# Optimization experiments

Hardware: AMD Instinct MI355X
Metric: run time of the kernel (lower is better)

The kernel has to match this reference:

```python
import jax, jax.numpy as jnp
import numpy as np

# Production-scale dims (GraspNet-style CloudCrop)
B, N, C, NS = 8, 1024, 256, 32          # batch, seed points (= npoint), feat dim, nsample
RADIUS, HMIN, HMAX = 0.05, -0.02, 0.04
EPS = 1e-5


def setup_inputs() -> dict:
    key = jax.random.key(0)
    ks = jax.random.split(key, 8)
    # seed points in a 0.2m cube -> cylinder of r=0.05, h=0.06 holds ~60 pts on avg
    seed_xyz_graspable = jax.random.uniform(ks[0], (B, N, 3), dtype=jnp.float32) * 0.2
    seed_features_graspable = jax.random.normal(ks[1], (B, C, N), dtype=jnp.float32)
    # random proper-ish rotation matrices via batched QR (orthonormal columns)
    q, _ = jnp.linalg.qr(jax.random.normal(ks[2], (B, N, 3, 3), dtype=jnp.float32))
    vp_rot = q
    cin = 3 + C
    # kaiming_normal for 1x1 convs (fan_in = cin), BN -> no conv bias
    W1 = jax.random.normal(ks[3], (256, cin), dtype=jnp.float32) * np.sqrt(2.0 / cin)
    W2 = jax.random.normal(ks[4], (256, 256), dtype=jnp.float32) * np.sqrt(2.0 / 256)
    g1 = jnp.ones((256,), jnp.float32); b1 = jnp.zeros((256,), jnp.float32)
    g2 = jnp.ones((256,), jnp.float32); b2 = jnp.zeros((256,), jnp.float32)
    return dict(seed_xyz_graspable=seed_xyz_graspable,
                seed_features_graspable=seed_features_graspable,
                vp_rot=vp_rot, W1=W1, g1=g1, b1=b1, W2=W2, g2=g2, b2=b2)


def _cylinder_query_idx(xyz, new_xyz, rot):
    # local coords: x_rot = R^T (p - c); rot flattened row-major in the original,
    # so local_k = sum_m rot[m, k] * diff_m  ==  einsum(diff, rot)
    diff = xyz[:, None, :, :] - new_xyz[:, :, None, :]          # (B, P, N, 3)
    local = jnp.einsum('bpnm,bpmk->bpnk', diff, rot)            # (B, P, N, 3)
    d2 = local[..., 1] ** 2 + local[..., 2] ** 2
    mask = (d2 < RADIUS ** 2) & (local[..., 0] > HMIN) & (local[..., 0] < HMAX)
    # first NS in-cylinder indices in original point order; empty slots -> index 0
    order = jnp.argsort(~mask, axis=-1)[..., :NS]               # stable sort
    valid = jnp.take_along_axis(mask, order, axis=-1)
    return jnp.where(valid, order, 0)                           # (B, P, NS) int32


def _conv_bn_relu(x, W, g, b):
    # 1x1 conv as channel GEMM, BatchNorm2d (training stats), ReLU
    y = jnp.einsum('bcps,oc->bops', x, W)                       # (B, O, P, S)
    mu = y.mean(axis=(0, 2, 3), keepdims=True)
    var = y.var(axis=(0, 2, 3), keepdims=True)
    y = (y - mu) * jax.lax.rsqrt(var + EPS)
    y = y * g[None, :, None, None] + b[None, :, None, None]
    return jax.nn.relu(y)


def reference(seed_xyz_graspable, seed_features_graspable, vp_rot,
              W1, g1, b1, W2, g2, b2):
    xyz, feats, rot = seed_xyz_graspable, seed_features_graspable, vp_rot
    idx = _cylinder_query_idx(xyz, xyz, rot)                    # centers == seeds
    # group xyz: gather, recenter, normalize by radius, rotate into cylinder frame
    gx = jax.vmap(lambda p, i: p[i])(xyz, idx)                  # (B, P, NS, 3)
    gx = (gx - xyz[:, :, None, :]) / RADIUS
    gx = jnp.einsum('bpsm,bpmk->bpsk', gx, rot)                 # rotate_xyz
    gf = jax.vmap(lambda f, i: f[:, i])(feats, idx)             # (B, C, P, NS)
    x = jnp.concatenate([gx.transpose(0, 3, 1, 2), gf], axis=1)  # (B, 3+C, P, NS)
    x = _conv_bn_relu(x, W1, g1, b1)
    x = _conv_bn_relu(x, W2, g2, b2)
    return x.max(axis=-1)                                        # (B, 256, P)
```

## Files before the change

kernel.cpp:

```cpp
#include <hip/hip_runtime.h>
#include <hip/hip_bf16.h>

#define DB 8
#define DN 1024
#define DP 1024
#define DC 256
#define DNS 32
#define DBP (DB * DP)
#define K1 288
#define K2 256
#define XS 296
#define YS 258
#define ROWS 128
#define NG (DBP / 4)
#define NK1 (K1 / 32)
#define NK2 (K2 / 32)

constexpr float kRadius = 0.05f;
constexpr float kR2 = kRadius * kRadius;
constexpr float kHmin = -0.02f;
constexpr float kHmax = 0.04f;
constexpr float kEps = 1e-5f;
constexpr float kInvCnt = 1.0f / (float)(DB * DP * DNS);

typedef __bf16 bf16x8 __attribute__((ext_vector_type(8)));
typedef float f32x4 __attribute__((ext_vector_type(4)));
static_assert(sizeof(bf16x8) == 16, "bf16x8 must be 16B");

constexpr size_t OF_FEATST = 0;
constexpr size_t OF_W1B  = OF_FEATST + (size_t)DB * DN * DC / 2;
constexpr size_t OF_W2B  = OF_W1B + (size_t)DC * K1 / 2;
constexpr size_t OF_IDX  = OF_W2B + (size_t)DC * K2 / 2;
constexpr size_t OF_GX   = OF_IDX + (size_t)DBP * DNS;
constexpr size_t OF_PART = OF_GX + (size_t)DBP * DNS * 3;
constexpr size_t OF_YMAX = OF_PART + (size_t)DBP * DC * 2;
constexpr size_t OF_YMIN = OF_YMAX + (size_t)DBP * DC;
constexpr size_t OF_BN1  = OF_YMIN + (size_t)DBP * DC;
constexpr size_t OF_BN2  = OF_BN1 + 512;
constexpr size_t OF_CNTZ = OF_BN2 + 512;
constexpr size_t OF_GWZ  = OF_CNTZ + (size_t)64 * DN;
constexpr size_t OF_GG64 = OF_GWZ + (size_t)64 * 3 * DN;
constexpr size_t OF_YPRT = OF_GG64 + 1024;

__device__ inline ushort f2b(float x) {
  union { __hip_bfloat16 h; ushort u; } c;
  c.h = __float2bfloat16(x);
  return c.u;
}
__device__ inline float b2f(ushort u) {
  union { uint u; float f; } c;
  c.u = (uint)u << 16;
  return c.f;
}

__global__ __launch_bounds__(256)
void k_prep(const float* __restrict__ f, uint* __restrict__ ftb,
            const float* __restrict__ W1, ushort* __restrict__ W1b,
            const float* __restrict__ W2, ushort* __restrict__ W2b) {
  __shared__ float t[32][33];
  int blk = blockIdx.x;
  int tid = threadIdx.x;
  if (blk < 2048) {
    int ct = blk & 7, nt = (blk >> 3) & 31, b = blk >> 8;
    int tx = tid & 31, ty = tid >> 5;
#pragma unroll
    for (int k = 0; k < 4; ++k) {
      int c = ct * 32 + ty + k * 8;
      t[ty + k * 8][tx] = f[((size_t)b * DC + c) * DN + nt * 32 + tx];
    }
    __syncthreads();
    uint* dst = ftb + (size_t)b * DN * (DC / 2);
#pragma unroll
    for (int it = 0; it < 2; ++it) {
      int idx = it * 256 + tid;
      int nl = idx >> 4, cp = idx & 15;
      uint v = (uint)f2b(t[2 * cp][nl]) | ((uint)f2b(t[2 * cp + 1][nl]) << 16);
      dst[(size_t)(nt * 32 + nl) * (DC / 2) + ct * 16 + cp] = v;
    }
  } else if (blk < 2336) {
    int gid = (blk - 2048) * 256 + tid;
    if (gid < DC * K1) {
      int o = gid / K1, kp = gid - o * K1;
      float v = 0.f;
      if (kp < 256) v = W1[o * 259 + 3 + kp];
      else if (kp < 259) v = W1[o * 259 + (kp - 256)];
      W1b[gid] = f2b(v);
    }
  } else {
    int gid = (blk - 2336) * 256 + tid;
    if (gid < DC * K2) W2b[gid] = f2b(W2[gid]);
  }
}

__global__ void k_query(const float* __restrict__ xyz, const float* __restrict__ rot,
                        int* __restrict__ idxp, float* __restrict__ gxp) {
  int bp = blockIdx.x;
  int b = bp >> 10;
  int lane = threadIdx.x;
  __shared__ int sidx[DNS];
  __shared__ float srot[9], sc[3];
  if (lane < DNS) sidx[lane] = 0;
  if (lane < 9) srot[lane] = rot[(size_t)bp * 9 + lane];
  if (lane < 3) sc[lane] = xyz[(size_t)bp * 3 + lane];
  __syncthreads();
  float r00 = srot[0], r01 = srot[1], r02 = srot[2];
  float r10 = srot[3], r11 = srot[4], r12 = srot[5];
  float r20 = srot[6], r21 = srot[7], r22 = srot[8];
  float cx = sc[0], cy = sc[1], cz = sc[2];
  const float* xb = xyz + (size_t)b * DN * 3;
  int cnt = 0;
  for (int ch = 0; ch < DN / 64 && cnt < DNS; ++ch) {
    int n = ch * 64 + lane;
    float dx = xb[n * 3 + 0] - cx, dy = xb[n * 3 + 1] - cy, dz = xb[n * 3 + 2] - cz;
    float lx = dx * r00 + dy * r10 + dz * r20;
    float ly = dx * r01 + dy * r11 + dz * r21;
    float lz = dx * r02 + dy * r12 + dz * r22;
    bool m = (ly * ly + lz * lz < kR2) && (lx > kHmin) && (lx < kHmax);
    unsigned long long bal = __ballot(m);
    int rank = cnt + __popcll(bal & ((1ull << lane) - 1ull));
    if (m && rank < DNS) sidx[rank] = n;
    cnt += __popcll(bal);
  }
  __syncthreads();
  if (lane < DNS) {
    int j = sidx[lane];
    idxp[(size_t)bp * DNS + lane] = j;
    float gx = (xb[j * 3 + 0] - cx) / kRadius;
    float gy = (xb[j * 3 + 1] - cy) / kRadius;
    float gz = (xb[j * 3 + 2] - cz) / kRadius;
    float* gp = gxp + ((size_t)bp * DNS + lane) * 3;
    gp[0] = gx * r00 + gy * r10 + gz * r20;
    gp[1] = gx * r01 + gy * r11 + gz * r21;
    gp[2] = gx * r02 + gy * r12 + gz * r22;
  }
}

__global__ __launch_bounds__(256)
void k_count(const int* __restrict__ idxp, const float* __restrict__ gxp,
             float* __restrict__ cntz, float* __restrict__ gwz,
             float* __restrict__ gg64) {
  __shared__ float h0[DN], h1[DN], h2[DN], h3[DN];
  int t = threadIdx.x;
  int blk = blockIdx.x;
  int b = blk >> 3, s = blk & 7;
  for (int i = t; i < DN; i += 256) {
    h0[i] = 0.f; h1[i] = 0.f; h2[i] = 0.f; h3[i] = 0.f;
  }
  __syncthreads();
  float p[9] = {0.f, 0.f, 0.f, 0.f, 0.f, 0.f, 0.f, 0.f, 0.f};
#pragma unroll
  for (int r = 0; r < 16; ++r) {
    int sid = blk * 4096 + r * 256 + t;
    int j = idxp[sid];
    const float* g = gxp + (size_t)sid * 3;
    float g0 = g[0], g1 = g[1], g2 = g[2];
    atomicAdd(&h0[j], 1.f);
    atomicAdd(&h1[j], g0);
    atomicAdd(&h2[j], g1);
    atomicAdd(&h3[j], g2);
    p[0] += g0 * g0; p[1] += g0 * g1; p[2] += g0 * g2;
    p[3] += g1 * g1; p[4] += g1 * g2; p[5] += g2 * g2;
    p[6] += g0; p[7] += g1; p[8] += g2;
  }
  __syncthreads();
  for (int i = t; i < DN; i += 256) {
    cntz[((size_t)b * 8 + s) * DN + i] = h0[i];
    gwz[(((size_t)b * 8 + s) * 3 + 0) * DN + i] = h1[i];
    gwz[(((size_t)b * 8 + s) * 3 + 1) * DN + i] = h2[i];
    gwz[(((size_t)b * 8 + s) * 3 + 2) * DN + i] = h3[i];
  }
  __shared__ float sgg[4][9];
#pragma unroll
  for (int v = 0; v < 9; ++v) {
    float sv = p[v];
#pragma unroll
    for (int m = 1; m < 64; m <<= 1) sv += __shfl_xor(sv, m, 64);
    if ((t & 63) == 0) sgg[t >> 6][v] = sv;
  }
  __syncthreads();
  if (t < 9) gg64[blk * 16 + t] = sgg[0][t] + sgg[1][t] + sgg[2][t] + sgg[3][t];
}

__global__ __launch_bounds__(256)
void k_ygemm(const uint4* __restrict__ ftb, const ushort* __restrict__ W1b,
             const float* __restrict__ W1, const float* __restrict__ cntz,
             const float* __restrict__ gwz, float2* __restrict__ ypart) {
  __shared__ ushort x_lds[ROWS * XS];
  __shared__ float c_lds[ROWS];
  __shared__ float g_lds[3][ROWS];
  __shared__ float wg_lds[DC][3];

  const int nb = blockIdx.x;
  const int b = nb >> 3;
  const int n0 = (nb & 7) * ROWS;
  const int tid = threadIdx.x;
  const int lane = tid & 63;
  const int wv = tid >> 6;
  const int l15 = lane & 15;
  const int l4 = lane >> 4;

  {
    const uint4* src = ftb + ((size_t)b * DN + n0) * (DC / 8);
    for (int idx = tid; idx < ROWS * 32; idx += 256) {
      int rrow = idx >> 5, col = idx & 31;
      ((uint4*)(x_lds + (size_t)rrow * XS))[col] = src[rrow * 32 + col];
    }
  }
  if (tid < ROWS) {
    float c = 0.f, g0 = 0.f, g1 = 0.f, g2 = 0.f;
#pragma unroll
    for (int s = 0; s < 8; ++s) {
      c += cntz[((size_t)b * 8 + s) * DN + n0 + tid];
      g0 += gwz[(((size_t)b * 8 + s) * 3 + 0) * DN + n0 + tid];
      g1 += gwz[(((size_t)b * 8 + s) * 3 + 1) * DN + n0 + tid];
      g2 += gwz[(((size_t)b * 8 + s) * 3 + 2) * DN + n0 + tid];
    }
    c_lds[tid] = c; g_lds[0][tid] = g0; g_lds[1][tid] = g1; g_lds[2][tid] = g2;
  }
  {
    wg_lds[tid][0] = W1[tid * 259 + 0];
    wg_lds[tid][1] = W1[tid * 259 + 1];
    wg_lds[tid][2] = W1[tid * 259 + 2];
  }
  __syncthreads();

  f32x4 acc[4][8];
#pragma unroll
  for (int t = 0; t < 4; ++t)
#pragma unroll
    for (int st = 0; st < 8; ++st)
#pragma unroll
      for (int r = 0; r < 4; ++r) acc[t][st][r] = 0.f;

  const int o0 = wv * 64;
  const ushort* xbase = x_lds + (size_t)l15 * XS + l4 * 8;
  {
    const ushort* wrow[4];
#pragma unroll
    for (int t = 0; t < 4; ++t)
      wrow[t] = W1b + (size_t)(o0 + t * 16 + l15) * K1 + l4 * 8;
#pragma unroll
    for (int ks = 0; ks < 8; ++ks) {
      bf16x8 bx[8], aw[4];
#pragma unroll
      for (int st = 0; st < 8; ++st)
        bx[st] = *(const bf16x8*)(xbase + (size_t)st * 16 * XS + ks * 32);
#pragma unroll
      for (int t = 0; t < 4; ++t) aw[t] = *(const bf16x8*)(wrow[t] + ks * 32);
#pragma unroll
      for (int st = 0; st < 8; ++st)
#pragma unroll
        for (int t = 0; t < 4; ++t)
          acc[t][st] = __builtin_amdgcn_mfma_f32_16x16x32_bf16(aw[t], bx[st],
                                                               acc[t][st], 0, 0, 0);
    }
  }

  float cn[8], h0[8], h1[8], h2[8];
#pragma unroll
  for (int st = 0; st < 8; ++st) {
    int n = st * 16 + l15;
    cn[st] = c_lds[n]; h0[st] = g_lds[0][n]; h1[st] = g_lds[1][n]; h2[st] = g_lds[2][n];
  }
#pragma unroll
  for (int t = 0; t < 4; ++t) {
#pragma unroll
    for (int r = 0; r < 4; ++r) {
      int o = o0 + t * 16 + l4 * 4 + r;
      float wg0 = wg_lds[o][0], wg1 = wg_lds[o][1], wg2 = wg_lds[o][2];
      float s = 0.f, q = 0.f;
#pragma unroll
      for (int st = 0; st < 8; ++st) {
        float Y = acc[t][st][r];
        float h = wg0 * h0[st] + wg1 * h1[st] + wg2 * h2[st];
        s = fmaf(cn[st], Y, s);
        q += cn[st] * Y * Y + 2.f * Y * h;
      }
#pragma unroll
      for (int m = 1; m < 16; m <<= 1) {
        s += __shfl_xor(s, m, 64);
        q += __shfl_xor(q, m, 64);
      }
      if (l15 == 0) ypart[(size_t)nb * DC + o] = make_float2(s, q);
    }
  }
}

__global__ __launch_bounds__(256)
void k_bn1f(const float2* __restrict__ ypart, const float* __restrict__ gg64,
            const float* __restrict__ W1, const float* __restrict__ gam,
            const float* __restrict__ bet, float* __restrict__ bn) {
  __shared__ float ggs[9];
  int t = threadIdx.x;
  if (t < 9) {
    float s = 0.f;
    for (int blk = 0; blk < 64; ++blk) s += gg64[blk * 16 + t];
    ggs[t] = s;
  }
  __syncthreads();
  float s = 0.f, q = 0.f;
  for (int nb = 0; nb < 64; ++nb) {
    float2 v = ypart[(size_t)nb * DC + t];
    s += v.x; q += v.y;
  }
  float wg0 = W1[t * 259 + 0], wg1 = W1[t * 259 + 1], wg2 = W1[t * 259 + 2];
  s += wg0 * ggs[6] + wg1 * ggs[7] + wg2 * ggs[8];
  q += wg0 * wg0 * ggs[0] + 2.f * wg0 * wg1 * ggs[1] + 2.f * wg0 * wg2 * ggs[2] +
       wg1 * wg1 * ggs[3] + 2.f * wg1 * wg2 * ggs[4] + wg2 * wg2 * ggs[5];
  float mu = s * kInvCnt;
  float var = q * kInvCnt - mu * mu;
  var = var < 0.f ? 0.f : var;
  float sc = gam[t] * rsqrtf(var + kEps);
  bn[t] = sc;
  bn[DC + t] = bet[t] - mu * sc;
}

__global__ __launch_bounds__(256, 2)
void k_gemm_full(const uint4* __restrict__ ftb, const ushort* __restrict__ W1b,
                 const ushort* __restrict__ W2b, const int* __restrict__ idxp,
                 const float* __restrict__ gxp, const float* __restrict__ bn1,
                 float2* __restrict__ part, float* __restrict__ ymax,
                 float* __restrict__ ymin) {
  __shared__ ushort x_lds[ROWS * XS];
  __shared__ float bn_lds[2 * DC];

  const int grp = blockIdx.x;
  const int bp0 = grp * 4;
  const int b = bp0 >> 10;
  const int tid = threadIdx.x;
  const int lane = tid & 63;
  const int wv = tid >> 6;
  const int l15 = lane & 15;
  const int l4 = lane >> 4;

  for (int i = tid; i < 2 * DC; i += 256) bn_lds[i] = bn1[i];

  {
    int q = tid & 7;
#pragma unroll
    for (int rep = 0; rep < 4; ++rep) {
      int s = (tid >> 3) + rep * 32;
      int j = idxp[(size_t)bp0 * DNS + s];
      const uint4* src = ftb + (size_t)(b * DN + j) * (DC / 8);
      uint4* dst = (uint4*)(x_lds + (size_t)s * XS);
#pragma unroll
      for (int k = 0; k < 4; ++k) dst[q + 8 * k] = src[q + 8 * k];
    }
  }
  if (tid < ROWS) {
    const float* g = gxp + ((size_t)bp0 * DNS + tid) * 3;
    uint a0 = (uint)f2b(g[0]) | ((uint)f2b(g[1]) << 16);
    uint a1 = (uint)f2b(g[2]);
    uint4* drow = (uint4*)(x_lds + (size_t)tid * XS + 256);
    drow[0] = make_uint4(a0, a1, 0u, 0u);
    drow[1] = make_uint4(0u, 0u, 0u, 0u);
    drow[2] = make_uint4(0u, 0u, 0u, 0u);
    drow[3] = make_uint4(0u, 0u, 0u, 0u);
  }
  __syncthreads();

  f32x4 acc[4][8];
#pragma unroll
  for (int t = 0; t < 4; ++t)
#pragma unroll
    for (int st = 0; st < 8; ++st)
#pragma unroll
      for (int r = 0; r < 4; ++r) acc[t][st][r] = 0.f;

  const int o0 = wv * 64;
  const ushort* xbase = x_lds + (size_t)l15 * XS + l4 * 8;

  {
    const ushort* wrow[4];
#pragma unroll
    for (int t = 0; t < 4; ++t)
      wrow[t] = W1b + (size_t)(o0 + t * 16 + l15) * K1 + l4 * 8;
    bf16x8 aw[4];
#pragma unroll
    for (int t = 0; t < 4; ++t) aw[t] = *(const bf16x8*)(wrow[t]);
#pragma unroll
    for (int ks = 0; ks < NK1; ++ks) {
      bf16x8 bx[8];
#pragma unroll
      for (int st = 0; st < 8; ++st)
        bx[st] = *(const bf16x8*)(xbase + (size_t)st * 16 * XS + ks * 32);
      bf16x8 an[4];
      if (ks + 1 < NK1) {
#pragma unroll
        for (int t = 0; t < 4; ++t)
          an[t] = *(const bf16x8*)(wrow[t] + (ks + 1) * 32);
      }
      __builtin_amdgcn_s_setprio(1);
#pragma unroll
      for (int st = 0; st < 8; ++st)
#pragma unroll
        for (int t = 0; t < 4; ++t)
          acc[t][st] = __builtin_amdgcn_mfma_f32_16x16x32_bf16(aw[t], bx[st],
                                                               acc[t][st], 0, 0, 0);
      __builtin_amdgcn_s_setprio(0);
      if (ks + 1 < NK1) {
#pragma unroll
        for (int t = 0; t < 4; ++t) aw[t] = an[t];
      }
    }
  }

  __syncthreads();
#pragma unroll
  for (int t = 0; t < 4; ++t) {
    int ob = o0 + t * 16 + l4 * 4;
    float sc0 = bn_lds[ob + 0], sh0 = bn_lds[DC + ob + 0];
    float sc1 = bn_lds[ob + 1], sh1 = bn_lds[DC + ob + 1];
    float sc2 = bn_lds[ob + 2], sh2 = bn_lds[DC + ob + 2];
    float sc3 = bn_lds[ob + 3], sh3 = bn_lds[DC + ob + 3];
#pragma unroll
    for (int st = 0; st < 8; ++st) {
      float v0 = fmaxf(fmaf(acc[t][st][0], sc0, sh0), 0.f);
      float v1 = fmaxf(fmaf(acc[t][st][1], sc1, sh1), 0.f);
      float v2 = fmaxf(fmaf(acc[t][st][2], sc2, sh2), 0.f);
      float v3 = fmaxf(fmaf(acc[t][st][3], sc3, sh3), 0.f);
      uint2 pk = make_uint2((uint)f2b(v0) | ((uint)f2b(v1) << 16),
                            (uint)f2b(v2) | ((uint)f2b(v3) << 16));
      int s = st * 16 + l15;
      *(uint2*)(x_lds + (size_t)s * XS + ob) = pk;
      acc[t][st][0] = 0.f; acc[t][st][1] = 0.f;
      acc[t][st][2] = 0.f; acc[t][st][3] = 0.f;
    }
  }
  __syncthreads();

  {
    const ushort* wrow[4];
#pragma unroll
    for (int t = 0; t < 4; ++t)
      wrow[t] = W2b + (size_t)(o0 + t * 16 + l15) * K2 + l4 * 8;
    bf16x8 aw[4];
#pragma unroll
    for (int t = 0; t < 4; ++t) aw[t] = *(const bf16x8*)(wrow[t]);
#pragma unroll
    for (int ks = 0; ks < NK2; ++ks) {
      bf16x8 bx[8];
#pragma unroll
      for (int st = 0; st < 8; ++st)
        bx[st] = *(const bf16x8*)(xbase + (size_t)st * 16 * XS + ks * 32);
      bf16x8 an[4];
      if (ks + 1 < NK2) {
#pragma unroll
        for (int t = 0; t < 4; ++t)
          an[t] = *(const bf16x8*)(wrow[t] + (ks + 1) * 32);
      }
      __builtin_amdgcn_s_setprio(1);
#pragma unroll
      for (int st = 0; st < 8; ++st)
#pragma unroll
        for (int t = 0; t < 4; ++t)
          acc[t][st] = __builtin_amdgcn_mfma_f32_16x16x32_bf16(aw[t], bx[st],
                                                               acc[t][st], 0, 0, 0);
      __builtin_amdgcn_s_setprio(0);
      if (ks + 1 < NK2) {
#pragma unroll
        for (int t = 0; t < 4; ++t) aw[t] = an[t];
      }
    }
  }

  __syncthreads();
#pragma unroll
  for (int t = 0; t < 4; ++t) {
    int ob = o0 + t * 16 + l4 * 4;
#pragma unroll
    for (int st = 0; st < 8; ++st) {
      uint2 pk = make_uint2(
          (uint)f2b(acc[t][st][0]) | ((uint)f2b(acc[t][st][1]) << 16),
          (uint)f2b(acc[t][st][2]) | ((uint)f2b(acc[t][st][3]) << 16));
      int s = st * 16 + l15;
      *(uint2*)(x_lds + (size_t)s * YS + ob) = pk;
    }
  }
  __syncthreads();
  {
    const ushort* col = x_lds + tid;
    float s = 0.f, q = 0.f;
#pragma unroll
    for (int p = 0; p < 4; ++p) {
      float mx = -3.4e38f, mn = 3.4e38f;
#pragma unroll 8
      for (int i = 0; i < DNS; ++i) {
        float v = b2f(col[(size_t)(p * DNS + i) * YS]);
        s += v; q += v * v;
        mx = fmaxf(mx, v); mn = fminf(mn, v);
      }
      ymax[(size_t)(bp0 + p) * DC + tid] = mx;
      ymin[(size_t)(bp0 + p) * DC + tid] = mn;
    }
    part[(size_t)grp * DC + tid] = make_float2(s, q);
  }
}

__global__ void k_reduce_bn(const float* __restrict__ part, const float* __restrict__ gam,
                            const float* __restrict__ bet, float* __restrict__ bn) {
  int o = blockIdx.x, tid = threadIdx.x;
  __shared__ float ss[256], sq[256];
  float s = 0.f, q = 0.f;
  const float2* pp = (const float2*)part;
  for (int g = tid; g < NG; g += 256) {
    float2 v = pp[(size_t)g * DC + o];
    s += v.x; q += v.y;
  }
  ss[tid] = s; sq[tid] = q;
  __syncthreads();
  for (int w = 128; w > 0; w >>= 1) {
    if (tid < w) { ss[tid] += ss[tid + w]; sq[tid] += sq[tid + w]; }
    __syncthreads();
  }
  if (tid == 0) {
    float mu = ss[0] * kInvCnt;
    float var = sq[0] * kInvCnt - mu * mu;
    var = var < 0.f ? 0.f : var;
    float sc = gam[o] * rsqrtf(var + kEps);
    bn[o] = sc;
    bn[DC + o] = bet[o] - mu * sc;
  }
}

__global__ void k_final(const float* __restrict__ ymax, const float* __restrict__ ymin,
                        const float* __restrict__ bn2, float* __restrict__ out) {
  __shared__ float tmax[32][33], tmin[32][33];
  int ot = blockIdx.x, pt = blockIdx.y, b = blockIdx.z;
  int tx = threadIdx.x, ty = threadIdx.y;
#pragma unroll
  for (int k = 0; k < 4; ++k) {
    int pr = ty + k * 8;
    size_t base = ((size_t)(b * DP) + pt * 32 + pr) * DC + ot * 32 + tx;
    tmax[pr][tx] = ymax[base];
    tmin[pr][tx] = ymin[base];
  }
  __syncthreads();
#pragma unroll
  for (int k = 0; k < 4; ++k) {
    int oc = ty + k * 8;
    int o = ot * 32 + oc;
    float sc = bn2[o], sh = bn2[DC + o];
    float m = (sc >= 0.f) ? tmax[tx][oc] : tmin[tx][oc];
    float v = fmaf(sc, m, sh);
    v = v > 0.f ? v : 0.f;
    out[((size_t)(b * DC) + o) * DP + pt * 32 + tx] = v;
  }
}

extern "C" void kernel_launch(void* const* d_in, const int* in_sizes, int n_in,
                              void* d_out, int out_size, void* d_ws, size_t ws_size,
                              hipStream_t stream) {
  const float* xyz   = (const float*)d_in[0];
  const float* feats = (const float*)d_in[1];
  const float* rot   = (const float*)d_in[2];
  const float* W1    = (const float*)d_in[3];
  const float* g1    = (const float*)d_in[4];
  const float* b1    = (const float*)d_in[5];
  const float* W2    = (const float*)d_in[6];
  const float* g2    = (const float*)d_in[7];
  const float* b2    = (const float*)d_in[8];
  float* out = (float*)d_out;

  float* ws = (float*)d_ws;
  uint*   ftb_u  = (uint*)(ws + OF_FEATST);
  uint4*  ftb    = (uint4*)(ws + OF_FEATST);
  ushort* W1b    = (ushort*)(ws + OF_W1B);
  ushort* W2b    = (ushort*)(ws + OF_W2B);
  int*    idxp   = (int*)(ws + OF_IDX);
  float*  gxp    = ws + OF_GX;
  float2* partp  = (float2*)(ws + OF_PART);
  float*  ymaxp  = ws + OF_YMAX;
  float*  yminp  = ws + OF_YMIN;
  float*  bn1p   = ws + OF_BN1;
  float*  bn2p   = ws + OF_BN2;
  float*  cntzp  = ws + OF_CNTZ;
  float*  gwzp   = ws + OF_GWZ;
  float*  gg64p  = ws + OF_GG64;
  float2* yprtp  = (float2*)(ws + OF_YPRT);

  k_prep<<<2592, 256, 0, stream>>>(feats, ftb_u, W1, W1b, W2, W2b);
  k_query<<<DBP, 64, 0, stream>>>(xyz, rot, idxp, gxp);

  k_count<<<64, 256, 0, stream>>>(idxp, gxp, cntzp, gwzp, gg64p);
  k_ygemm<<<64, 256, 0, stream>>>(ftb, W1b, W1, cntzp, gwzp, yprtp);
  k_bn1f<<<1, 256, 0, stream>>>(yprtp, gg64p, W1, g1, b1, bn1p);

  k_gemm_full<<<NG, 256, 0, stream>>>(ftb, W1b, W2b, idxp, gxp, bn1p, partp,
                                      ymaxp, yminp);
  k_reduce_bn<<<DC, 256, 0, stream>>>((const float*)partp, g2, b2, bn2p);
  k_final<<<dim3(DC / 32, DP / 32, DB), dim3(32, 8), 0, stream>>>(ymaxp, yminp, bn2p, out);
}
```

Baseline: 159.5 us.

## Split GEMM work across eight waves and pack four queries per block

The fused GEMM kernel now runs 512 threads per block. Each wave computes 32 output channels instead of 64, which halves accumulator registers per thread and aims for higher occupancy. The final per-channel column reduction is split across two halves and combined through LDS. The cylinder query kernel now processes four seed points per 256-thread block, one per wave, with per-wave shared arrays and no block barriers. This reduces launch and block-scheduling overhead but relies on wave-level LDS ordering.

```diff
diff --git a/kernel.cpp b/kernel.cpp
--- a/kernel.cpp
+++ b/kernel.cpp
@@ -92,21 +92,22 @@
   }
 }
 
-__global__ void k_query(const float* __restrict__ xyz, const float* __restrict__ rot,
-                        int* __restrict__ idxp, float* __restrict__ gxp) {
-  int bp = blockIdx.x;
+__global__ __launch_bounds__(256)
+void k_query(const float* __restrict__ xyz, const float* __restrict__ rot,
+             int* __restrict__ idxp, float* __restrict__ gxp) {
+  int wv = threadIdx.x >> 6;
+  int lane = threadIdx.x & 63;
+  int bp = blockIdx.x * 4 + wv;
   int b = bp >> 10;
-  int lane = threadIdx.x;
-  __shared__ int sidx[DNS];
-  __shared__ float srot[9], sc[3];
-  if (lane < DNS) sidx[lane] = 0;
-  if (lane < 9) srot[lane] = rot[(size_t)bp * 9 + lane];
-  if (lane < 3) sc[lane] = xyz[(size_t)bp * 3 + lane];
-  __syncthreads();
-  float r00 = srot[0], r01 = srot[1], r02 = srot[2];
-  float r10 = srot[3], r11 = srot[4], r12 = srot[5];
-  float r20 = srot[6], r21 = srot[7], r22 = srot[8];
-  float cx = sc[0], cy = sc[1], cz = sc[2];
+  __shared__ int sidx[4][DNS];
+  __shared__ float srot[4][9], sc[4][3];
+  if (lane < DNS) sidx[wv][lane] = 0;
+  if (lane < 9) srot[wv][lane] = rot[(size_t)bp * 9 + lane];
+  if (lane < 3) sc[wv][lane] = xyz[(size_t)bp * 3 + lane];
+  float r00 = srot[wv][0], r01 = srot[wv][1], r02 = srot[wv][2];
+  float r10 = srot[wv][3], r11 = srot[wv][4], r12 = srot[wv][5];
+  float r20 = srot[wv][6], r21 = srot[wv][7], r22 = srot[wv][8];
+  float cx = sc[wv][0], cy = sc[wv][1], cz = sc[wv][2];
   const float* xb = xyz + (size_t)b * DN * 3;
   int cnt = 0;
   for (int ch = 0; ch < DN / 64 && cnt < DNS; ++ch) {
@@ -118,12 +119,11 @@
     bool m = (ly * ly + lz * lz < kR2) && (lx > kHmin) && (lx < kHmax);
     unsigned long long bal = __ballot(m);
     int rank = cnt + __popcll(bal & ((1ull << lane) - 1ull));
-    if (m && rank < DNS) sidx[rank] = n;
+    if (m && rank < DNS) sidx[wv][rank] = n;
     cnt += __popcll(bal);
   }
-  __syncthreads();
   if (lane < DNS) {
-    int j = sidx[lane];
+    int j = sidx[wv][lane];
     idxp[(size_t)bp * DNS + lane] = j;
     float gx = (xb[j * 3 + 0] - cx) / kRadius;
     float gy = (xb[j * 3 + 1] - cy) / kRadius;
@@ -315,7 +315,7 @@
   bn[DC + t] = bet[t] - mu * sc;
 }
 
-__global__ __launch_bounds__(256, 2)
+__global__ __launch_bounds__(512, 4)
 void k_gemm_full(const uint4* __restrict__ ftb, const ushort* __restrict__ W1b,
                  const ushort* __restrict__ W2b, const int* __restrict__ idxp,
                  const float* __restrict__ gxp, const float* __restrict__ bn1,
@@ -333,13 +333,13 @@
   const int l15 = lane & 15;
   const int l4 = lane >> 4;
 
-  for (int i = tid; i < 2 * DC; i += 256) bn_lds[i] = bn1[i];
+  bn_lds[tid] = bn1[tid];
 
   {
     int q = tid & 7;
 #pragma unroll
-    for (int rep = 0; rep < 4; ++rep) {
-      int s = (tid >> 3) + rep * 32;
+    for (int rep = 0; rep < 2; ++rep) {
+      int s = (tid >> 3) + rep * 64;
       int j = idxp[(size_t)bp0 * DNS + s];
       const uint4* src = ftb + (size_t)(b * DN + j) * (DC / 8);
       uint4* dst = (uint4*)(x_lds + (size_t)s * XS);
@@ -359,55 +359,55 @@
   }
   __syncthreads();
 
-  f32x4 acc[4][8];
-#pragma unroll
-  for (int t = 0; t < 4; ++t)
+  f32x4 acc[2][8];
+#pragma unroll
+  for (int t = 0; t < 2; ++t)
 #pragma unroll
     for (int st = 0; st < 8; ++st)
 #pragma unroll
       for (int r = 0; r < 4; ++r) acc[t][st][r] = 0.f;
 
-  const int o0 = wv * 64;
+  const int o0 = wv * 32;
   const ushort* xbase = x_lds + (size_t)l15 * XS + l4 * 8;
 
   {
-    const ushort* wrow[4];
-#pragma unroll
-    for (int t = 0; t < 4; ++t)
+    const ushort* wrow[2];
+#pragma unroll
+    for (int t = 0; t < 2; ++t)
       wrow[t] = W1b + (size_t)(o0 + t * 16 + l15) * K1 + l4 * 8;
-    bf16x8 aw[4];
-#pragma unroll
-    for (int t = 0; t < 4; ++t) aw[t] = *(const bf16x8*)(wrow[t]);
+    bf16x8 aw[2];
+#pragma unroll
+    for (int t = 0; t < 2; ++t) aw[t] = *(const bf16x8*)(wrow[t]);
 #pragma unroll
     for (int ks = 0; ks < NK1; ++ks) {
       bf16x8 bx[8];
 #pragma unroll
       for (int st = 0; st < 8; ++st)
         bx[st] = *(const bf16x8*)(xbase + (size_t)st * 16 * XS + ks * 32);
-      bf16x8 an[4];
+      bf16x8 an[2];
       if (ks + 1 < NK1) {
 #pragma unroll
-        for (int t = 0; t < 4; ++t)
+        for (int t = 0; t < 2; ++t)
           an[t] = *(const bf16x8*)(wrow[t] + (ks + 1) * 32);
       }
       __builtin_amdgcn_s_setprio(1);
 #pragma unroll
       for (int st = 0; st < 8; ++st)
 #pragma unroll
-        for (int t = 0; t < 4; ++t)
+        for (int t = 0; t < 2; ++t)
           acc[t][st] = __builtin_amdgcn_mfma_f32_16x16x32_bf16(aw[t], bx[st],
                                                                acc[t][st], 0, 0, 0);
       __builtin_amdgcn_s_setprio(0);
       if (ks + 1 < NK1) {
 #pragma unroll
-        for (int t = 0; t < 4; ++t) aw[t] = an[t];
+        for (int t = 0; t < 2; ++t) aw[t] = an[t];
       }
     }
   }
 
   __syncthreads();
 #pragma unroll
-  for (int t = 0; t < 4; ++t) {
+  for (int t = 0; t < 2; ++t) {
     int ob = o0 + t * 16 + l4 * 4;
     float sc0 = bn_lds[ob + 0], sh0 = bn_lds[DC + ob + 0];
     float sc1 = bn_lds[ob + 1], sh1 = bn_lds[DC + ob + 1];
@@ -430,43 +430,43 @@
   __syncthreads();
 
   {
-    const ushort* wrow[4];
-#pragma unroll
-    for (int t = 0; t < 4; ++t)
+    const ushort* wrow[2];
+#pragma unroll
+    for (int t = 0; t < 2; ++t)
       wrow[t] = W2b + (size_t)(o0 + t * 16 + l15) * K2 + l4 * 8;
-    bf16x8 aw[4];
-#pragma unroll
-    for (int t = 0; t < 4; ++t) aw[t] = *(const bf16x8*)(wrow[t]);
+    bf16x8 aw[2];
+#pragma unroll
+    for (int t = 0; t < 2; ++t) aw[t] = *(const bf16x8*)(wrow[t]);
 #pragma unroll
     for (int ks = 0; ks < NK2; ++ks) {
       bf16x8 bx[8];
 #pragma unroll
       for (int st = 0; st < 8; ++st)
         bx[st] = *(const bf16x8*)(xbase + (size_t)st * 16 * XS + ks * 32);
-      bf16x8 an[4];
+      bf16x8 an[2];
       if (ks + 1 < NK2) {
 #pragma unroll
-        for (int t = 0; t < 4; ++t)
+        for (int t = 0; t < 2; ++t)
           an[t] = *(const bf16x8*)(wrow[t] + (ks + 1) * 32);
       }
       __builtin_amdgcn_s_setprio(1);
 #pragma unroll
       for (int st = 0; st < 8; ++st)
 #pragma unroll
-        for (int t = 0; t < 4; ++t)
+        for (int t = 0; t < 2; ++t)
           acc[t][st] = __builtin_amdgcn_mfma_f32_16x16x32_bf16(aw[t], bx[st],
                                                                acc[t][st], 0, 0, 0);
       __builtin_amdgcn_s_setprio(0);
       if (ks + 1 < NK2) {
 #pragma unroll
-        for (int t = 0; t < 4; ++t) aw[t] = an[t];
+        for (int t = 0; t < 2; ++t) aw[t] = an[t];
       }
     }
   }
 
   __syncthreads();
 #pragma unroll
-  for (int t = 0; t < 4; ++t) {
+  for (int t = 0; t < 2; ++t) {
     int ob = o0 + t * 16 + l4 * 4;
 #pragma unroll
     for (int st = 0; st < 8; ++st) {
@@ -479,10 +479,13 @@
   }
   __syncthreads();
   {
-    const ushort* col = x_lds + tid;
+    float* redp = (float*)(x_lds + (size_t)ROWS * YS);
+    int o = tid & 255, half = tid >> 8;
+    const ushort* col = x_lds + o;
     float s = 0.f, q = 0.f;
 #pragma unroll
-    for (int p = 0; p < 4; ++p) {
+    for (int p2 = 0; p2 < 2; ++p2) {
+      int p = half * 2 + p2;
       float mx = -3.4e38f, mn = 3.4e38f;
 #pragma unroll 8
       for (int i = 0; i < DNS; ++i) {
@@ -490,10 +493,17 @@
         s += v; q += v * v;
         mx = fmaxf(mx, v); mn = fminf(mn, v);
       }
-      ymax[(size_t)(bp0 + p) * DC + tid] = mx;
-      ymin[(size_t)(bp0 + p) * DC + tid] = mn;
-    }
-    part[(size_t)grp * DC + tid] = make_float2(s, q);
+      ymax[(size_t)(bp0 + p) * DC + o] = mx;
+      ymin[(size_t)(bp0 + p) * DC + o] = mn;
+    }
+    redp[half * 256 + o] = s;
+    redp[512 + half * 256 + o] = q;
+    __syncthreads();
+    if (tid < 256) {
+      float ss = redp[tid] + redp[256 + tid];
+      float qq = redp[512 + tid] + redp[768 + tid];
+      part[(size_t)grp * DC + tid] = make_float2(ss, qq);
+    }
   }
 }
 
@@ -580,13 +590,13 @@
   float2* yprtp  = (float2*)(ws + OF_YPRT);
 
   k_prep<<<2592, 256, 0, stream>>>(feats, ftb_u, W1, W1b, W2, W2b);
-  k_query<<<DBP, 64, 0, stream>>>(xyz, rot, idxp, gxp);
+  k_query<<<DBP / 4, 256, 0, stream>>>(xyz, rot, idxp, gxp);
 
   k_count<<<64, 256, 0, stream>>>(idxp, gxp, cntzp, gwzp, gg64p);
   k_ygemm<<<64, 256, 0, stream>>>(ftb, W1b, W1, cntzp, gwzp, yprtp);
   k_bn1f<<<1, 256, 0, stream>>>(yprtp, gg64p, W1, g1, b1, bn1p);
 
-  k_gemm_full<<<NG, 256, 0, stream>>>(ftb, W1b, W2b, idxp, gxp, bn1p, partp,
+  k_gemm_full<<<NG, 512, 0, stream>>>(ftb, W1b, W2b, idxp, gxp, bn1p, partp,
                                       ymaxp, yminp);
   k_reduce_bn<<<DC, 256, 0, stream>>>((const float*)partp, g2, b2, bn2p);
   k_final<<<dim3(DC / 32, DP / 32, DB), dim3(32, 8), 0, stream>>>(ymaxp, yminp, bn2p, out);
```

Result: no change. 158.5 us (-0.6%).
